# Kernel tuning notes

Measured on AMD Instinct MI355X. Metric: run time of the kernel, lower is better.

Reference implementation:

```python
import jax, jax.numpy as jnp
from jax import lax
import numpy as np

MAX_D = 4  # max_displacement


def conv3x3(x, w, b):
    # x: [B,Cin,H,W], w: [Cout,Cin,3,3], SAME padding (pad=1)
    y = lax.conv_general_dilated(
        x, w, window_strides=(1, 1), padding='SAME',
        dimension_numbers=('NCHW', 'OIHW', 'NCHW'))
    return y + b[None, :, None, None]


def compute_cost_volume(f1, f2, d):
    # roll+mask in the torch code == shift with zero padding:
    # cv[idx,h,w] = mean_c f1[c,h,w] * f2[c,h-i,w-j] (zero outside bounds)
    B, C, H, W = f1.shape
    pad = jnp.pad(f2, ((0, 0), (0, 0), (d, d), (d, d)))
    slices = []
    for i in range(-d, d + 1):
        for j in range(-d, d + 1):
            shifted = lax.dynamic_slice(pad, (0, 0, d - i, d - j), (B, C, H, W))
            slices.append((f1 * shifted).sum(axis=1) / C)  # [B,H,W]
    return jnp.stack(slices, axis=1)  # [B,81,H,W]


def setup_inputs() -> dict:
    key = jax.random.key(0)
    ks = jax.random.split(key, 10)
    B, C, H, W = 16, 64, 128, 128
    cv_ch = (2 * MAX_D + 1) ** 2  # 81
    def w_init(k, shape):
        fan_in = shape[1] * shape[2] * shape[3]
        return jax.random.normal(k, shape, dtype=jnp.float32) * np.float32(np.sqrt(2.0 / fan_in))
    return {
        'f1': jax.random.normal(ks[0], (B, C, H, W), dtype=jnp.float32),
        'f2_warped': jax.random.normal(ks[1], (B, C, H, W), dtype=jnp.float32),
        'w1': w_init(ks[2], (128, C + cv_ch, 3, 3)),
        'b1': jnp.zeros((128,), dtype=jnp.float32),
        'w2': w_init(ks[3], (64, 128, 3, 3)),
        'b2': jnp.zeros((64,), dtype=jnp.float32),
        'w3': w_init(ks[4], (32, 64, 3, 3)),
        'b3': jnp.zeros((32,), dtype=jnp.float32),
        'w4': w_init(ks[5], (2, 32, 3, 3)),
        'b4': jnp.zeros((2,), dtype=jnp.float32),
    }


def reference(f1, f2_warped, w1, b1, w2, b2, w3, b3, w4, b4):
    cv = compute_cost_volume(f1, f2_warped, MAX_D)       # [B,81,H,W]
    x = jnp.concatenate([f1, cv], axis=1)                # [B,145,H,W]
    x = jax.nn.relu(conv3x3(x, w1, b1))
    x = jax.nn.relu(conv3x3(x, w2, b2))
    x = jax.nn.relu(conv3x3(x, w3, b3))
    flow = conv3x3(x, w4, b4)                            # [B,2,H,W]
    return flow
```

## Files before the change

### kernel.cpp

```cpp
#include <hip/hip_runtime.h>


typedef __bf16 bf16x8 __attribute__((ext_vector_type(8)));
typedef float f32x4 __attribute__((ext_vector_type(4)));

__device__ __forceinline__ unsigned short f2bf_bits(float f) {
  unsigned int u = __float_as_uint(f);
  unsigned int r = (u + 0x7FFFu + ((u >> 16) & 1u)) >> 16;
  return (unsigned short)r;
}

__device__ __forceinline__ void glds16(const ushort* gp, ushort* lp) {
  __builtin_amdgcn_global_load_lds((const __attribute__((address_space(1))) void*)gp,
                                   (__attribute__((address_space(3))) void*)lp, 16, 0, 0);
}

__global__ void prep_w_kernel(const float* __restrict__ w, uint4* __restrict__ wp,
                              int CIN, int COUT, int CHUNKS, int NFRAG) {
  int idx = blockIdx.x * 256 + threadIdx.x;
  int total = CHUNKS * 9 * NFRAG * 64;
  if (idx >= total) return;
  int lane = idx & 63;
  int fi = idx >> 6;
  int nf = fi % NFRAG;
  int t = fi / NFRAG;
  int rs = t % 9;
  int c = t / 9;
  int co = nf * 16 + (lane & 15);
  int cib = c * 32 + (lane >> 4) * 8;
  union { uint4 q; ushort s[8]; } pk;
#pragma unroll
  for (int e = 0; e < 8; ++e) {
    int ci = cib + e;
    float v = (ci < CIN && co < COUT) ? w[(co * CIN + ci) * 9 + rs] : 0.f;
    pk.s[e] = f2bf_bits(v);
  }
  wp[idx] = pk.q;
}

__global__ __launch_bounds__(256) void pack_f1_kernel(const float* __restrict__ f1,
                                                      ushort* __restrict__ xf1) {
  __shared__ float tile[64][132];
  const int bid = blockIdx.x;
  const int h = bid & 127, b = bid >> 7;
  const int tid = threadIdx.x;
  for (int e = tid; e < 64 * 128; e += 256) {
    int c = e >> 7, w = e & 127;
    tile[c][w] = f1[((b * 64 + c) * 128 + h) * 128 + w];
  }
  __syncthreads();
  const int px = tid >> 1, cgb = (tid & 1) * 4;
  const long base = ((long)(b * 128 + h) * 128 + px) * 64;
#pragma unroll
  for (int e = 0; e < 4; ++e) {
    int c0 = (cgb + e) * 8;
    union { uint4 q; ushort s[8]; } pk;
#pragma unroll
    for (int k = 0; k < 8; ++k) pk.s[k] = f2bf_bits(tile[c0 + k][px]);
    *reinterpret_cast<uint4*>(&xf1[base + c0]) = pk.q;
  }
}

__global__ __launch_bounds__(256)
void cost_volume_mfma_kernel(const ushort* __restrict__ xf1,
                             const ushort* __restrict__ xf2,
                             ushort* __restrict__ xcv) {
  const int bx = blockIdx.x;
  const int idx = bx >> 3;
  const int b = 2 * (bx & 7) + (idx >> 7);
  const int h = idx & 127;
  const int tid = threadIdx.x;
  const int lane = tid & 63;
  const int g = tid >> 6;
  const int l15 = lane & 15;
  const int lg = lane >> 4;

  __shared__ __align__(16) float sC[4][2][16][33];
  __shared__ __align__(16) ushort sO[96][132];

  {
    uint4 z = make_uint4(0u, 0u, 0u, 0u);
    uint4* p = (uint4*)sO;
#pragma unroll
    for (int j = 0; j < 7; ++j) {
      int e = tid + j * 256;
      if (e < 1584) p[e] = z;
    }
  }
  __syncthreads();

  const int w0g = g * 32;
  bf16x8 afr[2][2];
  {
    const ushort* f1p = xf1 + ((long)(b * 128 + h) * 128) * 64;
#pragma unroll
    for (int wt = 0; wt < 2; ++wt)
#pragma unroll
      for (int kc = 0; kc < 2; ++kc) {
        int pix = w0g + wt * 16 + l15;
        afr[wt][kc] = *reinterpret_cast<const bf16x8*>(f1p + pix * 64 + kc * 32 + lg * 8);
      }
  }

  const float inv = 1.0f / 64.0f;
  for (int A = 0; A < 9; ++A) {
    int fr = h - 4 + A;
    if ((unsigned)fr >= 128u) continue;
    const ushort* f2p = xf2 + ((long)(b * 128 + fr) * 128) * 64;
    bf16x8 bfr[3][2];
#pragma unroll
    for (int t = 0; t < 3; ++t)
#pragma unroll
      for (int kc = 0; kc < 2; ++kc) {
        int p = w0g - 4 + t * 16 + l15;
        uint4 v = make_uint4(0u, 0u, 0u, 0u);
        if ((unsigned)p < 128u)
          v = *reinterpret_cast<const uint4*>(f2p + (long)p * 64 + kc * 32 + lg * 8);
        bfr[t][kc] = __builtin_bit_cast(bf16x8, v);
      }
#pragma unroll
    for (int wt = 0; wt < 2; ++wt)
#pragma unroll
      for (int nt = 0; nt < 2; ++nt) {
        f32x4 acc = {0.f, 0.f, 0.f, 0.f};
        acc = __builtin_amdgcn_mfma_f32_16x16x32_bf16(afr[wt][0], bfr[wt + nt][0], acc, 0, 0, 0);
        acc = __builtin_amdgcn_mfma_f32_16x16x32_bf16(afr[wt][1], bfr[wt + nt][1], acc, 0, 0, 0);
#pragma unroll
        for (int j = 0; j < 4; ++j)
          sC[g][wt][lg * 4 + j][nt * 16 + l15] = acc[j];
      }
    const int chb = (8 - A) * 9;
#pragma unroll
    for (int wt = 0; wt < 2; ++wt) {
      int px = w0g + wt * 16 + l15;
#pragma unroll
      for (int u = 0; u < 3; ++u) {
        if (u < ((lg == 3) ? 3 : 2)) {
          int tj = lg * 2 + u;
          float v = sC[g][wt][l15][l15 + 8 - tj];
          sO[chb + tj][px] = f2bf_bits(v * inv);
        }
      }
    }
  }
  __syncthreads();

  uint4* dst = reinterpret_cast<uint4*>(xcv + ((long)(b * 128 + h) * 128) * 96);
#pragma unroll
  for (int j = 0; j < 6; ++j) {
    int t8 = j * 256 + tid;
    int px = t8 / 12;
    int ch0 = (t8 - px * 12) * 8;
    union { uint4 qq; ushort ss[8]; } pk;
#pragma unroll
    for (int k = 0; k < 8; ++k) pk.ss[k] = sO[ch0 + k][px];
    dst[t8] = pk.qq;
  }
}

template <int CA, int CB, int COUT, bool RELU, bool PLANAR>
__global__ __launch_bounds__(512, 2)
void conv_mfma_kernel(const ushort* __restrict__ xa, const ushort* __restrict__ xb,
                      const uint4* __restrict__ wp, const float* __restrict__ bias,
                      void* __restrict__ outv) {
  constexpr int CHUNKS = (CA + CB) / 32;
  constexpr int NFRAG = COUT / 16;
  constexpr int NFW = (NFRAG >= 2) ? NFRAG / 2 : 1;
  constexpr int MFW = (NFRAG >= 2) ? 4 : 2;
  constexpr int SXN = 4 * 130 * 32;
  constexpr int WTQ = 9 * NFRAG * 64;
  constexpr int WTA_Q = 5 * NFRAG * 64;
  constexpr int WTB_Q = 4 * NFRAG * 64;
  constexpr int WIA = (WTA_Q + 511) / 512;
  constexpr int WIB = (WTB_Q + 511) / 512;
  constexpr int SO_STRIDE = COUT + 4;
  constexpr int STAGE_B = PLANAR ? 2048 : 2 * 128 * SO_STRIDE * 2;
  constexpr int SX_B = 2 * SXN * 2;
  constexpr int BASE_B = SX_B + (WTA_Q + WTB_Q) * 16;
  constexpr int ARENA_B = STAGE_B > BASE_B ? STAGE_B : BASE_B;

  __shared__ __align__(16) char arena[ARENA_B];
  ushort* sXa = (ushort*)arena;
  ushort* sWtA = (ushort*)(arena + SX_B);
  ushort* sWtB = (ushort*)(arena + SX_B + WTA_Q * 16);

  const int bx = blockIdx.x;
  const int idx = bx >> 3;
  const int b = 2 * (bx & 7) + (idx >> 6);
  const int h0 = (idx & 63) * 2;
  const int tid = threadIdx.x;
  const int lane = tid & 63;
  const int wid = tid >> 6;
  const int l15 = lane & 15;
  const int lg = lane >> 4;
  const int cg    = (NFRAG >= 2) ? (wid >> 2) : 0;
  const int row   = (NFRAG >= 2) ? ((wid >> 1) & 1) : (wid >> 2);
  const int pbase = (NFRAG >= 2) ? ((wid & 1) * 64) : ((wid & 3) * 32);

  f32x4 acc[MFW][NFW];
#pragma unroll
  for (int mf = 0; mf < MFW; ++mf)
#pragma unroll
    for (int nf = 0; nf < NFW; ++nf) acc[mf][nf] = {0.f, 0.f, 0.f, 0.f};

  if (tid < 64) {
    int bi = tid >> 5, tr = (tid >> 3) & 3, wz = (tid >> 2) & 1, gq = tid & 3;
    int wl = wz ? 129 : 0;
    *reinterpret_cast<uint4*>(&sXa[bi * SXN + ((tr * 130 + wl) * 4 + gq) * 8]) =
        make_uint4(0u, 0u, 0u, 0u);
  }
  if (h0 == 0 || h0 == 126) {
    const int trz = (h0 == 0) ? 0 : 3;
#pragma unroll
    for (int e = 0; e < 2; ++e) {
      int u = tid + e * 512;
      int bi = u >> 9, k = u & 511;
      *reinterpret_cast<uint4*>(&sXa[bi * SXN + ((trz * 130 + 1) * 4 + k) * 8]) =
          make_uint4(0u, 0u, 0u, 0u);
    }
  }

  auto stage = [&](int c, int bi) {
    const int c0 = c * 32;
    const ushort* src;
    int cst, coff;
    if (CB == 0 || c0 < CA) { src = xa; cst = CA; coff = c0; }
    else                    { src = xb; cst = CB; coff = c0 - CA; }
    const int tr = wid >> 1;
    const int gh = h0 - 1 + tr;
    if ((unsigned)gh < 128u) {
      const ushort* rowp = src + ((long)(b * 128 + gh) * 128) * cst + coff;
#pragma unroll
      for (int t = 0; t < 4; ++t) {
        int s = (wid & 1) * 4 + t;
        int u = s * 64 + lane;
        int wl = 1 + (u >> 2);
        int gq = lane & 3;
        int sw = (wl + (wl >> 2)) & 3;
        const ushort* gp = rowp + (long)(wl - 1) * cst + (gq ^ sw) * 8;
        ushort* lp = &sXa[bi * SXN + ((tr * 130 + 1) * 4 + s * 64) * 8];
        glds16(gp, lp);
      }
    }
  };

  auto stage_wtA = [&](int c) {
    const ushort* src = (const ushort*)(wp + (size_t)c * WTQ);
#pragma unroll
    for (int i = 0; i < WIA; ++i) {
      int e = tid + i * 512;
      if ((WTA_Q % 512) == 0 || e < WTA_Q)
        glds16(src + (size_t)e * 8, sWtA + (size_t)(tid & ~63) * 8 + (size_t)(i * 512) * 8);
    }
  };
  auto stage_wtB = [&](int c) {
    const ushort* src = (const ushort*)(wp + (size_t)c * WTQ + WTA_Q);
#pragma unroll
    for (int i = 0; i < WIB; ++i) {
      int e = tid + i * 512;
      if ((WTB_Q % 512) == 0 || e < WTB_Q)
        glds16(src + (size_t)e * 8, sWtB + (size_t)(tid & ~63) * 8 + (size_t)(i * 512) * 8);
    }
  };

  auto compute = [&](int bi, int rs0, int rs1, const ushort* wbuf) {
#pragma unroll
    for (int rs = rs0; rs < rs1; ++rs) {
      const int r = rs / 3, s = rs % 3;
      const int tr = row + r;
      bf16x8 afr[MFW];
#pragma unroll
      for (int mf = 0; mf < MFW; ++mf) {
        int wl = pbase + mf * 16 + l15 + s;
        int sw = (wl + (wl >> 2)) & 3;
        afr[mf] = *reinterpret_cast<const bf16x8*>(
            &sXa[bi * SXN + ((tr * 130 + wl) * 4 + (lg ^ sw)) * 8]);
      }
      const ushort* wrow = wbuf + (size_t)((rs - rs0) * NFRAG + cg * NFW) * 64 * 8;
#pragma unroll
      for (int nf = 0; nf < NFW; ++nf) {
        bf16x8 bfr = *reinterpret_cast<const bf16x8*>(wrow + (nf * 64 + lane) * 8);
#pragma unroll
        for (int mf = 0; mf < MFW; ++mf)
          acc[mf][nf] = __builtin_amdgcn_mfma_f32_16x16x32_bf16(afr[mf], bfr, acc[mf][nf], 0, 0, 0);
      }
    }
  };

  stage(0, 0);
  stage_wtA(0);
  __syncthreads();

  for (int c = 0; c < CHUNKS; ++c) {
    const int bi = c & 1;
    if (c + 1 < CHUNKS) stage(c + 1, (c + 1) & 1);
    stage_wtB(c);
    compute(bi, 0, 5, sWtA);
    __syncthreads();
    if (c + 1 < CHUNKS) stage_wtA(c + 1);
    compute(bi, 5, 9, sWtB);
    __syncthreads();
  }

  if (!PLANAR) {
    ushort* sO = (ushort*)arena;
#pragma unroll
    for (int nf = 0; nf < NFW; ++nf) {
      float bs = bias[cg * NFW * 16 + nf * 16 + l15];
#pragma unroll
      for (int mf = 0; mf < MFW; ++mf) {
        int px2 = row * 128 + pbase + mf * 16 + lg * 4;
#pragma unroll
        for (int j = 0; j < 4; ++j) {
          float v = acc[mf][nf][j] + bs;
          if (RELU) v = fmaxf(v, 0.f);
          sO[(px2 + j) * SO_STRIDE + cg * NFW * 16 + nf * 16 + l15] = f2bf_bits(v);
        }
      }
    }
    __syncthreads();
    constexpr int QPP = COUT / 8;
    uint4* dst = reinterpret_cast<uint4*>((ushort*)outv + ((long)(b * 128 + h0) * 128) * COUT);
#pragma unroll
    for (int t0 = 0; t0 < 2 * 128 * QPP / 512; ++t0) {
      int t = t0 * 512 + tid;
      int px2 = t / QPP;
      int ch0 = (t & (QPP - 1)) * 8;
      union { uint4 qq; ushort ss[8]; } pk;
#pragma unroll
      for (int k = 0; k < 8; ++k) pk.ss[k] = sO[px2 * SO_STRIDE + ch0 + k];
      dst[t] = pk.qq;
    }
  } else {
    float* sF = (float*)arena;
    if (l15 < 2) {
#pragma unroll
      for (int mf = 0; mf < MFW; ++mf) {
        int pxb = pbase + mf * 16 + lg * 4;
#pragma unroll
        for (int j = 0; j < 4; ++j)
          sF[(l15 * 2 + row) * 128 + pxb + j] = acc[mf][0][j] + bias[l15];
      }
    }
    __syncthreads();
    float* out = (float*)outv;
    if (tid < 128) {
      int ch = tid >> 6, r = (tid >> 5) & 1, qx = tid & 31;
      *reinterpret_cast<float4*>(&out[((long)(b * 2 + ch) * 128 + h0 + r) * 128 + qx * 4]) =
          *reinterpret_cast<float4*>(&sF[(ch * 2 + r) * 128 + qx * 4]);
    }
  }
}

extern "C" void kernel_launch(void* const* d_in, const int* in_sizes, int n_in,
                              void* d_out, int out_size, void* d_ws, size_t ws_size,
                              hipStream_t stream) {
  (void)in_sizes; (void)n_in; (void)out_size; (void)ws_size;
  const float* f1 = (const float*)d_in[0];
  const float* f2 = (const float*)d_in[1];
  const float* w1 = (const float*)d_in[2];
  const float* b1 = (const float*)d_in[3];
  const float* w2 = (const float*)d_in[4];
  const float* b2 = (const float*)d_in[5];
  const float* w3 = (const float*)d_in[6];
  const float* b3 = (const float*)d_in[7];
  const float* w4 = (const float*)d_in[8];
  const float* b4 = (const float*)d_in[9];

  char* ws = (char*)d_ws;
  size_t off = 0;
  ushort* xf1 = (ushort*)(ws + off); off += (size_t)262144 * 64 * 2;
  ushort* xcv = (ushort*)(ws + off); off += (size_t)262144 * 96 * 2;
  ushort* x1  = (ushort*)(ws + off); off += (size_t)262144 * 128 * 2;
  ushort* x2  = (ushort*)(ws + off); off += (size_t)262144 * 64 * 2;
  uint4* wp1 = (uint4*)(ws + off); off += (size_t)5 * 9 * 8 * 64 * 16;
  uint4* wp2 = (uint4*)(ws + off); off += (size_t)4 * 9 * 4 * 64 * 16;
  uint4* wp3 = (uint4*)(ws + off); off += (size_t)2 * 9 * 2 * 64 * 16;
  uint4* wp4 = (uint4*)(ws + off); off += (size_t)1 * 9 * 1 * 64 * 16;
  ushort* x3  = xf1;
  ushort* xf2 = x1;

  prep_w_kernel<<<90, 256, 0, stream>>>(w1, wp1, 145, 128, 5, 8);
  prep_w_kernel<<<36, 256, 0, stream>>>(w2, wp2, 128, 64, 4, 4);
  prep_w_kernel<<<9, 256, 0, stream>>>(w3, wp3, 64, 32, 2, 2);
  prep_w_kernel<<<3, 256, 0, stream>>>(w4, wp4, 32, 2, 1, 1);

  pack_f1_kernel<<<2048, 256, 0, stream>>>(f1, xf1);
  pack_f1_kernel<<<2048, 256, 0, stream>>>(f2, xf2);
  cost_volume_mfma_kernel<<<2048, 256, 0, stream>>>(xf1, xf2, xcv);

  conv_mfma_kernel<64, 96, 128, true, false><<<1024, 512, 0, stream>>>(xf1, xcv, wp1, b1, x1);
  conv_mfma_kernel<128, 0, 64, true, false><<<1024, 512, 0, stream>>>(x1, x1, wp2, b2, x2);
  conv_mfma_kernel<64, 0, 32, true, false><<<1024, 512, 0, stream>>>(x2, x2, wp3, b3, x3);
  conv_mfma_kernel<32, 0, 16, false, true><<<1024, 512, 0, stream>>>(x3, x3, wp4, b4, d_out);
}
```

Before: 309.0 us.

## Keep conv weights in registers streamed from global for the two largest convs

Adds a new conv kernel for the first two layers that streams weight fragments straight from global memory into registers, double-buffered across three kernel-row pieces, instead of staging them through LDS. It removes the LDS weight buffers and the extra barriers between weight stages, leaving LDS only for activations. It also reorders the activation prefetch after the weight staging in the existing kernel. The cost is higher register pressure and global or L2 weight traffic repeated for every block.

```diff
diff --git a/kernel.cpp b/kernel.cpp
--- a/kernel.cpp
+++ b/kernel.cpp
@@ -155,6 +155,168 @@
 #pragma unroll
     for (int k = 0; k < 8; ++k) pk.ss[k] = sO[ch0 + k][px];
     dst[t8] = pk.qq;
+  }
+}
+
+template <int CA, int CB, int COUT_TOTAL, int CGDIV, int MFW, bool RELU>
+__global__ __launch_bounds__(512, 2)
+void conv_wreg_kernel(const ushort* __restrict__ xa, const ushort* __restrict__ xb,
+                      const uint4* __restrict__ wp, const float* __restrict__ bias,
+                      ushort* __restrict__ out) {
+  constexpr int CHUNKS = (CA + CB) / 32;
+  constexpr int NFRAGT = COUT_TOTAL / 16;
+  constexpr int NFW = NFRAGT / CGDIV;
+  constexpr int SXN = 4 * 130 * 32;
+  constexpr int SX_B = 2 * SXN * 2;
+  constexpr int SO_B = 256 * (COUT_TOTAL + 4) * 2;
+  constexpr int ARENA_B = (SO_B > SX_B) ? SO_B : SX_B;
+
+  __shared__ __align__(16) char arena[ARENA_B];
+  ushort* sXa = (ushort*)arena;
+
+  const int bx = blockIdx.x;
+  const int idx = bx >> 3;
+  const int b = 2 * (bx & 7) + (idx >> 6);
+  const int h0 = (idx & 63) * 2;
+  const int tid = threadIdx.x;
+  const int lane = tid & 63;
+  const int wid = tid >> 6;
+  const int l15 = lane & 15;
+  const int lg = lane >> 4;
+  const int cg = (CGDIV == 2) ? (wid >> 2) : 0;
+  const int wrem = (CGDIV == 2) ? (wid & 3) : wid;
+  constexpr int PDIV = 128 / (MFW * 16);
+  const int row = wrem / PDIV;
+  const int pbase = (wrem % PDIV) * (MFW * 16);
+
+  f32x4 acc[MFW][4];
+#pragma unroll
+  for (int mf = 0; mf < MFW; ++mf)
+#pragma unroll
+    for (int nf = 0; nf < 4; ++nf) acc[mf][nf] = {0.f, 0.f, 0.f, 0.f};
+
+  if (tid < 64) {
+    int bi = tid >> 5, tr = (tid >> 3) & 3, wz = (tid >> 2) & 1, gq = tid & 3;
+    int wl = wz ? 129 : 0;
+    *reinterpret_cast<uint4*>(&sXa[bi * SXN + ((tr * 130 + wl) * 4 + gq) * 8]) =
+        make_uint4(0u, 0u, 0u, 0u);
+  }
+  if (h0 == 0 || h0 == 126) {
+    const int trz = (h0 == 0) ? 0 : 3;
+#pragma unroll
+    for (int e = 0; e < 2; ++e) {
+      int u = tid + e * 512;
+      int bi = u >> 9, k = u & 511;
+      *reinterpret_cast<uint4*>(&sXa[bi * SXN + ((trz * 130 + 1) * 4 + k) * 8]) =
+          make_uint4(0u, 0u, 0u, 0u);
+    }
+  }
+
+  auto stage_act = [&](int c, int bi) {
+    const int c0 = c * 32;
+    const ushort* src; int cst, coff;
+    if (CB == 0 || c0 < CA) { src = xa; cst = CA; coff = c0; }
+    else                    { src = xb; cst = CB; coff = c0 - CA; }
+    const int tr = wid >> 1;
+    const int gh = h0 - 1 + tr;
+    if ((unsigned)gh < 128u) {
+      const ushort* rowp = src + ((long)(b * 128 + gh) * 128) * cst + coff;
+#pragma unroll
+      for (int t = 0; t < 4; ++t) {
+        int s = (wid & 1) * 4 + t;
+        int u = s * 64 + lane;
+        int wl = 1 + (u >> 2);
+        int gq = lane & 3;
+        int sw = (wl + (wl >> 2)) & 3;
+        const ushort* gp = rowp + (long)(wl - 1) * cst + (gq ^ sw) * 8;
+        ushort* lp = &sXa[bi * SXN + ((tr * 130 + 1) * 4 + s * 64) * 8];
+        glds16(gp, lp);
+      }
+    }
+  };
+
+  auto load_piece = [&](uint4 (&dst)[12], int c, int p) {
+    const uint4* src = wp + ((size_t)(c * 9 + p * 3) * NFRAGT + cg * NFW) * 64 + lane;
+#pragma unroll
+    for (int rsl = 0; rsl < 3; ++rsl)
+#pragma unroll
+      for (int nf = 0; nf < 4; ++nf)
+        dst[rsl * 4 + nf] = src[(rsl * NFRAGT + nf) * 64];
+  };
+
+  auto compute_piece = [&](const uint4 (&wsrc)[12], int bi, int p) {
+    const int tr = row + p;
+#pragma unroll
+    for (int s = 0; s < 3; ++s) {
+      bf16x8 afr[MFW];
+#pragma unroll
+      for (int mf = 0; mf < MFW; ++mf) {
+        int wl = pbase + mf * 16 + l15 + s;
+        int sw = (wl + (wl >> 2)) & 3;
+        afr[mf] = *reinterpret_cast<const bf16x8*>(
+            &sXa[bi * SXN + ((tr * 130 + wl) * 4 + (lg ^ sw)) * 8]);
+      }
+#pragma unroll
+      for (int nf = 0; nf < 4; ++nf) {
+        bf16x8 bfr = __builtin_bit_cast(bf16x8, wsrc[s * 4 + nf]);
+#pragma unroll
+        for (int mf = 0; mf < MFW; ++mf)
+          acc[mf][nf] = __builtin_amdgcn_mfma_f32_16x16x32_bf16(afr[mf], bfr, acc[mf][nf], 0, 0, 0);
+      }
+    }
+  };
+
+  uint4 WA[12], WB[12];
+
+  auto chunk_body = [&](uint4 (&W0)[12], uint4 (&W1)[12], int c) {
+    const int bi = c & 1;
+    if (c + 1 < CHUNKS) stage_act(c + 1, bi ^ 1);
+    load_piece(W1, c, 1);
+    compute_piece(W0, bi, 0);
+    load_piece(W0, c, 2);
+    compute_piece(W1, bi, 1);
+    if (c + 1 < CHUNKS) load_piece(W1, c + 1, 0);
+    compute_piece(W0, bi, 2);
+    __syncthreads();
+  };
+
+  stage_act(0, 0);
+  load_piece(WA, 0, 0);
+  __syncthreads();
+
+  for (int c = 0; c < CHUNKS; ++c) {
+    if ((c & 1) == 0) chunk_body(WA, WB, c);
+    else              chunk_body(WB, WA, c);
+  }
+
+  constexpr int SO_STRIDE = COUT_TOTAL + 4;
+  ushort* sO = (ushort*)arena;
+#pragma unroll
+  for (int nf = 0; nf < 4; ++nf) {
+    float bs = bias[cg * 64 + nf * 16 + l15];
+#pragma unroll
+    for (int mf = 0; mf < MFW; ++mf) {
+      int px2 = row * 128 + pbase + mf * 16 + lg * 4;
+#pragma unroll
+      for (int j = 0; j < 4; ++j) {
+        float v = acc[mf][nf][j] + bs;
+        if (RELU) v = fmaxf(v, 0.f);
+        sO[(px2 + j) * SO_STRIDE + cg * 64 + nf * 16 + l15] = f2bf_bits(v);
+      }
+    }
+  }
+  __syncthreads();
+  constexpr int QPP = COUT_TOTAL / 8;
+  uint4* dst = reinterpret_cast<uint4*>(out + ((long)(b * 128 + h0) * 128) * COUT_TOTAL);
+#pragma unroll
+  for (int t0 = 0; t0 < 256 * QPP / 512; ++t0) {
+    int t = t0 * 512 + tid;
+    int px2 = t / QPP;
+    int ch0 = (t & (QPP - 1)) * 8;
+    union { uint4 qq; ushort ss[8]; } pk;
+#pragma unroll
+    for (int k = 0; k < 8; ++k) pk.ss[k] = sO[px2 * SO_STRIDE + ch0 + k];
+    dst[t] = pk.qq;
   }
 }
 
@@ -293,8 +455,8 @@
 
   for (int c = 0; c < CHUNKS; ++c) {
     const int bi = c & 1;
-    if (c + 1 < CHUNKS) stage(c + 1, (c + 1) & 1);
     stage_wtB(c);
+    if (c + 1 < CHUNKS) stage(c + 1, bi ^ 1);
     compute(bi, 0, 5, sWtA);
     __syncthreads();
     if (c + 1 < CHUNKS) stage_wtA(c + 1);
@@ -389,8 +551,8 @@
   pack_f1_kernel<<<2048, 256, 0, stream>>>(f2, xf2);
   cost_volume_mfma_kernel<<<2048, 256, 0, stream>>>(xf1, xf2, xcv);
 
-  conv_mfma_kernel<64, 96, 128, true, false><<<1024, 512, 0, stream>>>(xf1, xcv, wp1, b1, x1);
-  conv_mfma_kernel<128, 0, 64, true, false><<<1024, 512, 0, stream>>>(x1, x1, wp2, b2, x2);
+  conv_wreg_kernel<64, 96, 128, 2, 4, true><<<1024, 512, 0, stream>>>(xf1, xcv, wp1, b1, x1);
+  conv_wreg_kernel<128, 0, 64, 1, 2, true><<<1024, 512, 0, stream>>>(x1, x1, wp2, b2, x2);
   conv_mfma_kernel<64, 0, 32, true, false><<<1024, 512, 0, stream>>>(x2, x2, wp3, b3, x3);
   conv_mfma_kernel<32, 0, 16, false, true><<<1024, 512, 0, stream>>>(x3, x3, wp4, b4, d_out);
 }
```

After: 515.8 us. 1.67x slower.
